# Optimization experiments

Measured on AMD Instinct MI355X. Metric: run time of the kernel, lower is better.

The kernel has to match this reference:

```python
import jax, jax.numpy as jnp
import numpy as np

D_MODEL = 1024
RES = 45.0  # max_len / clamp resolution


def setup_inputs() -> dict:
    key = jax.random.key(0)
    # positions: scaled so clamping at +/-RES and both signs occur
    x = jax.random.normal(key, (2048, 32), dtype=jnp.float32) * 60.0
    return {"x": x}


def reference(x) -> jnp.ndarray:
    nbatch, nsources = x.shape
    d = D_MODEL
    # embs row 0: reversed arange (neg positions), row 1: arange (non-neg)
    embs = jnp.stack([jnp.arange(d - 1, -1, -1), jnp.arange(d)], axis=0).astype(jnp.float32)  # (2, d)
    # denom[r, j] = RES ** (2 * floor(embs[r, j] / 2) / d)
    denom = jnp.power(RES, 2.0 * jnp.floor(embs / 2.0) / d)  # (2, d)

    xc = jnp.clip(x, -RES, RES).reshape(nbatch * nsources)  # (N,)
    row = (xc >= 0).astype(jnp.int32)                        # (N,) selects embs row
    ang = jnp.abs(xc)[:, None] / denom[row]                  # (N, d)

    out = ang.at[:, 0::2].set(jnp.sin(ang[:, 0::2]))
    out = out.at[:, 1::2].set(jnp.cos(ang[:, 1::2]))
    return out.reshape(nbatch, nsources, d)
```

## Files before the change

kernel.cpp:

```cpp
#include <hip/hip_runtime.h>


#define PE_D 1024
#define PE_RES 45.0f

typedef float vfloat4 __attribute__((ext_vector_type(4)));

__global__ __launch_bounds__(256) void PositionalEncodingAngle_kernel(
    const float* __restrict__ x, float* __restrict__ out) {
    const int n = blockIdx.x;
    const int tid = threadIdx.x;

    const float v  = x[n];
    const float xc = fminf(fmaxf(v, -PE_RES), PE_RES);
    const float a  = fabsf(xc);
    const bool  pos = (xc >= 0.0f);

    const float c = 0.010726275578769f;

    const float k0    = pos ? (float)(2 * tid) : (float)(511 - 2 * tid);
    const float kstep = pos ? 1.0f : -1.0f;

    vfloat4 o;
    {
        const float ang = a * exp2f(-c * k0);
        o.x = __sinf(ang);
        o.y = __cosf(ang);
    }
    {
        const float ang = a * exp2f(-c * (k0 + kstep));
        o.z = __sinf(ang);
        o.w = __cosf(ang);
    }

    __builtin_nontemporal_store(o, reinterpret_cast<vfloat4*>(out) + (size_t)n * (PE_D / 4) + tid);
}

extern "C" void kernel_launch(void* const* d_in, const int* in_sizes, int n_in,
                              void* d_out, int out_size, void* d_ws, size_t ws_size,
                              hipStream_t stream) {
    const float* x = (const float*)d_in[0];
    float* out = (float*)d_out;
    const int N = out_size / PE_D;
    PositionalEncodingAngle_kernel<<<N, 256, 0, stream>>>(x, out);
}
```

Baseline: 267.3 us.

## Process 32 rows per block and precompute per-thread inverse denominators

Each block now handles 32 consecutive rows and computes the four per-column exp2 denominators once per thread, reusing them across rows and picking the sign-dependent pair with a select. This takes the exp2 calls out of the per-row work and cuts the grid from 65536 to 2048 blocks. The kernel is bound by output writes, so the saved ALU work may not matter much, and fewer blocks each doing a serial loop could reduce how many memory requests are in flight at once.

After: 264.5 us. About the same (-1.0%).

```diff
diff --git a/kernel.cpp b/kernel.cpp
--- a/kernel.cpp
+++ b/kernel.cpp
@@ -3,37 +3,45 @@
 
 #define PE_D 1024
 #define PE_RES 45.0f
+#define ROWS_PER_BLOCK 32
 
 typedef float vfloat4 __attribute__((ext_vector_type(4)));
 
 __global__ __launch_bounds__(256) void PositionalEncodingAngle_kernel(
-    const float* __restrict__ x, float* __restrict__ out) {
-    const int n = blockIdx.x;
+    const float* __restrict__ x, float* __restrict__ out, int N) {
     const int tid = threadIdx.x;
-
-    const float v  = x[n];
-    const float xc = fminf(fmaxf(v, -PE_RES), PE_RES);
-    const float a  = fabsf(xc);
-    const bool  pos = (xc >= 0.0f);
+    const int n0  = blockIdx.x * ROWS_PER_BLOCK;
 
     const float c = 0.010726275578769f;
+    const int   k0 = 2 * tid;
 
-    const float k0    = pos ? (float)(2 * tid) : (float)(511 - 2 * tid);
-    const float kstep = pos ? 1.0f : -1.0f;
+    const float e_pos0 = exp2f(-c * (float)(k0));
+    const float e_pos1 = exp2f(-c * (float)(k0 + 1));
+    const float e_neg0 = exp2f(-c * (float)(511 - k0));
+    const float e_neg1 = exp2f(-c * (float)(510 - k0));
 
-    vfloat4 o;
-    {
-        const float ang = a * exp2f(-c * k0);
-        o.x = __sinf(ang);
-        o.y = __cosf(ang);
+    const int n_end = (n0 + ROWS_PER_BLOCK < N) ? n0 + ROWS_PER_BLOCK : N;
+
+    for (int n = n0; n < n_end; ++n) {
+        const float v  = x[n];
+        const float xc = fminf(fmaxf(v, -PE_RES), PE_RES);
+        const float a  = fabsf(xc);
+        const bool  pos = (xc >= 0.0f);
+
+        const float d0 = pos ? e_pos0 : e_neg0;
+        const float d1 = pos ? e_pos1 : e_neg1;
+
+        const float ang0 = a * d0;
+        const float ang1 = a * d1;
+
+        vfloat4 o;
+        o.x = __sinf(ang0);
+        o.y = __cosf(ang0);
+        o.z = __sinf(ang1);
+        o.w = __cosf(ang1);
+
+        __builtin_nontemporal_store(o, reinterpret_cast<vfloat4*>(out) + (size_t)n * (PE_D / 4) + tid);
     }
-    {
-        const float ang = a * exp2f(-c * (k0 + kstep));
-        o.z = __sinf(ang);
-        o.w = __cosf(ang);
-    }
-
-    __builtin_nontemporal_store(o, reinterpret_cast<vfloat4*>(out) + (size_t)n * (PE_D / 4) + tid);
 }
 
 extern "C" void kernel_launch(void* const* d_in, const int* in_sizes, int n_in,
@@ -42,5 +50,6 @@
     const float* x = (const float*)d_in[0];
     float* out = (float*)d_out;
     const int N = out_size / PE_D;
-    PositionalEncodingAngle_kernel<<<N, 256, 0, stream>>>(x, out);
+    const int grid = (N + ROWS_PER_BLOCK - 1) / ROWS_PER_BLOCK;
+    PositionalEncodingAngle_kernel<<<grid, 256, 0, stream>>>(x, out, N);
 }
```
